# Performance work log

Hardware: AMD Instinct MI355X
Metric: run time of the kernel (lower is better)

Reference implementation:

```python
import jax, jax.numpy as jnp
import numpy as np

N, V, E, C_IN, C_OUT = 4, 4096, 2048, 64, 64


def setup_inputs() -> dict:
    key = jax.random.key(0)
    k_x, k_h, k_th = jax.random.split(key, 3)
    x = jax.random.normal(k_x, (N, V, C_IN), dtype=jnp.float32)
    H = (jax.random.uniform(k_h, (N, V, E)) < 0.05).astype(jnp.float32)
    # guarantee every vertex and every hyperedge has degree >= 1 (code divides by degree)
    v_idx = jnp.arange(V)
    H = H.at[:, v_idx, v_idx % E].set(1.0)
    # xavier_uniform for theta
    limit = float(np.sqrt(6.0 / (C_IN + C_OUT)))
    theta = jax.random.uniform(k_th, (C_IN, C_OUT), minval=-limit, maxval=limit, dtype=jnp.float32)
    bias = jnp.zeros((C_OUT,), dtype=jnp.float32)
    return {"x": x, "H": H, "theta": theta, "bias": bias}


def reference(x, H, theta, bias):
    # x: [N,V,C], H: [N,V,E] incidence, theta: [C,O], bias: [O]
    # Original builds diag_embed(1/deg) and multiplies; equivalent to direct
    # per-row / per-column scaling of H (same math, no NxVxV / NxExE diagonals).
    dv = 1.0 / H.sum(-1)            # [N,V] vertex degrees
    de = 1.0 / H.sum(1)             # [N,E] hyperedge degrees
    y = jnp.einsum('nvc,co->nvo', x, theta)          # [N,V,O]
    HDe = H * de[:, None, :]                          # H @ De  -> [N,V,E]
    y = jnp.einsum('nvc,nve->nec', y, HDe)            # vertex -> edge  [N,E,O]
    HDv = H * dv[:, :, None]                          # Dv @ H -> [N,V,E]
    y = jnp.einsum('nec,nve->nvc', y, HDv)            # edge -> vertex  [N,V,O]
    return y + bias[None, None, :]
```

## Files before the change

kernel.cpp:

```cpp
#include <hip/hip_runtime.h>
#include <hip/hip_bf16.h>
#include <stdint.h>

#define N_B 4
#define NV 4096
#define NE 2048
#define NC 64

typedef float    f32x4  __attribute__((ext_vector_type(4)));
typedef __bf16   bf16x8 __attribute__((ext_vector_type(8)));
typedef unsigned short u16;
typedef u16      u16x8  __attribute__((ext_vector_type(8)));
typedef uint32_t u32x4  __attribute__((ext_vector_type(4)));

__device__ __forceinline__ u16 f2bf_rne(float f) {
    uint32_t u = __builtin_bit_cast(uint32_t, f);
    u += 0x7FFFu + ((u >> 16) & 1u);
    return (u16)(u >> 16);
}
__device__ __forceinline__ float bf2f(u16 h) {
    uint32_t u = ((uint32_t)h) << 16;
    return __builtin_bit_cast(float, u);
}
__device__ __forceinline__ f32x4 mfma_bf16(u16x8 a, u16x8 b, f32x4 c) {
    return __builtin_amdgcn_mfma_f32_16x16x32_bf16(
        __builtin_bit_cast(bf16x8, a), __builtin_bit_cast(bf16x8, b), c, 0, 0, 0);
}
__device__ __forceinline__ u16x8 expand8(uint32_t byte) {
    u32x4 w;
#pragma unroll
    for (int p = 0; p < 4; ++p) {
        const uint32_t lo = (byte >> (2 * p)) & 1u;
        const uint32_t hi = (byte >> (2 * p + 1)) & 1u;
        w[p] = (lo | (hi << 16)) * 0x3F80u;
    }
    return __builtin_bit_cast(u16x8, w);
}

__global__ __launch_bounds__(256) void k_pack(const float* __restrict__ H,
                                              uint32_t* __restrict__ HB,
                                              uint32_t* __restrict__ HT,
                                              float* __restrict__ dvP,
                                              float* __restrict__ deP) {
    __shared__ float tile[64][65];
    const int n  = blockIdx.z;
    const int v0 = blockIdx.y * 64;
    const int e0 = blockIdx.x * 64;
    const int t = threadIdx.x, w = t >> 6, l = t & 63;

    const float* __restrict__ Hn = H + ((size_t)n * NV + v0) * NE + e0;

#pragma unroll 4
    for (int i = 0; i < 16; ++i) {
        const int row = w * 16 + i;
        const float h = Hn[(size_t)row * NE + l];
        tile[row][l] = h;
        const unsigned long long m = __ballot(h != 0.0f);
        if (l == 0)
            dvP[((size_t)blockIdx.x * N_B + n) * NV + v0 + row] = (float)__popcll(m);
        if (l < 2)
            HB[(((size_t)n * (NV / 16) + ((v0 + row) >> 4)) * (NE / 32) + (e0 >> 5) + l) * 16 +
               ((v0 + row) & 15)] = (uint32_t)(m >> (32 * l));
    }
    __syncthreads();

#pragma unroll 4
    for (int i = 0; i < 16; ++i) {
        const int col = w * 16 + i;
        const float h = tile[l][col];
        const unsigned long long m = __ballot(h != 0.0f);
        if (l == 0)
            deP[((size_t)blockIdx.y * N_B + n) * NE + e0 + col] = (float)__popcll(m);
        if (l < 2)
            HT[(((size_t)n * (NE / 16) + ((e0 + col) >> 4)) * (NV / 32) + (v0 >> 5) + l) * 16 +
               ((e0 + col) & 15)] = (uint32_t)(m >> (32 * l));
    }
}

__global__ __launch_bounds__(256) void k_deg(const float* __restrict__ dvP,
                                             const float* __restrict__ deP,
                                             float* __restrict__ dv,
                                             float* __restrict__ de) {
    const int id = blockIdx.x * 256 + threadIdx.x;
    if (id < N_B * NE) {
        float s = 0.f;
        for (int vt = 0; vt < 64; ++vt) s += deP[(size_t)vt * (N_B * NE) + id];
        de[id] = s;
    } else {
        const int j = id - N_B * NE;
        float s = 0.f;
        for (int et = 0; et < 32; ++et) s += dvP[(size_t)et * (N_B * NV) + j];
        dv[j] = s;
    }
}

__global__ __launch_bounds__(256) void k_xtheta(const float* __restrict__ x,
                                                const float* __restrict__ th,
                                                u16* __restrict__ Yh,
                                                u16* __restrict__ Yl) {
    __shared__ float xs[64][65];
    __shared__ float ts[64][65];
    const int t = threadIdx.x;
    const int n  = blockIdx.x >> 6;
    const int v0 = (blockIdx.x & 63) * 64;

#pragma unroll
    for (int i = 0; i < 4; ++i) {
        const int idx = i * 256 + t;
        const int row = idx >> 4, q = (idx & 15) * 4;
        const float4 xv = *(const float4*)&x[((size_t)(n * NV + v0 + row)) * 64 + q];
        const float4 tv = *(const float4*)&th[(size_t)row * 64 + q];
        xs[row][q] = xv.x; xs[row][q + 1] = xv.y; xs[row][q + 2] = xv.z; xs[row][q + 3] = xv.w;
        ts[row][q] = tv.x; ts[row][q + 1] = tv.y; ts[row][q + 2] = tv.z; ts[row][q + 3] = tv.w;
    }
    __syncthreads();

    const int v4 = (t & 15) * 4;
    const int c4 = (t >> 4) * 4;
    float acc[4][4] = {};
#pragma unroll
    for (int k = 0; k < 64; ++k) {
        float tv[4], xv[4];
#pragma unroll
        for (int i = 0; i < 4; ++i) { tv[i] = ts[k][c4 + i]; xv[i] = xs[v4 + i][k]; }
#pragma unroll
        for (int i = 0; i < 4; ++i)
#pragma unroll
            for (int j = 0; j < 4; ++j) acc[i][j] += tv[i] * xv[j];
    }
#pragma unroll
    for (int i = 0; i < 4; ++i) {
        ushort4 hi, lo;
        u16 h;
        h = f2bf_rne(acc[i][0]); hi.x = h; lo.x = f2bf_rne(acc[i][0] - bf2f(h));
        h = f2bf_rne(acc[i][1]); hi.y = h; lo.y = f2bf_rne(acc[i][1] - bf2f(h));
        h = f2bf_rne(acc[i][2]); hi.z = h; lo.z = f2bf_rne(acc[i][2] - bf2f(h));
        h = f2bf_rne(acc[i][3]); hi.w = h; lo.w = f2bf_rne(acc[i][3] - bf2f(h));
        const size_t o = ((size_t)n * 64 + c4 + i) * NV + v0 + v4;
        *(ushort4*)&Yh[o] = hi;
        *(ushort4*)&Yl[o] = lo;
    }
}

__global__ __launch_bounds__(256, 4) void k_v2e(const uint32_t* __restrict__ HT,
                                                const u16* __restrict__ Yh,
                                                const u16* __restrict__ Yl,
                                                float* __restrict__ P2) {
    const int n  = blockIdx.z;
    const int sp = blockIdx.y;
    const int e0 = blockIdx.x * 64;
    const int krange = NV / gridDim.y;
    const int kk0 = sp * krange;
    const int S   = krange / 32;

    const int t = threadIdx.x, w = t >> 6, l = t & 63;
    const int lq = l >> 4, lr = l & 15;
    const int sh = lq * 8;
    const int hstride = (NV / 32) * 16;

    const uint32_t* __restrict__ ht =
        HT + ((size_t)n * (NE / 16) + (e0 >> 4)) * hstride + (kk0 >> 5) * 16 + lr;
    const u16* __restrict__ ybh = Yh + ((size_t)n * 64 + w * 16 + lr) * NV + kk0 + lq * 8;
    const u16* __restrict__ ybl = Yl + ((size_t)n * 64 + w * 16 + lr) * NV + kk0 + lq * 8;

    f32x4 acc0 = {0.f,0.f,0.f,0.f}, acc1 = acc0, acc2 = acc0, acc3 = acc0;

    uint32_t A[4][4];
#pragma unroll
    for (int d = 0; d < 4; ++d) {
        A[d][0] = ht[0 * hstride + d * 16];
        A[d][1] = ht[1 * hstride + d * 16];
        A[d][2] = ht[2 * hstride + d * 16];
        A[d][3] = ht[3 * hstride + d * 16];
    }
    u16x8 BH[2], BL[2];
    BH[0] = *(const u16x8*)ybh;
    BL[0] = *(const u16x8*)ybl;

#define V2E_STEP(s, u, GUARD_A, GUARD_B)                                      \
    {                                                                         \
        const uint32_t a0 = A[u][0], a1 = A[u][1], a2 = A[u][2], a3 = A[u][3];\
        if (GUARD_A) {             \
            A[u][0] = ht[0 * hstride + ((s) + 4) * 16];                       \
            A[u][1] = ht[1 * hstride + ((s) + 4) * 16];                       \
            A[u][2] = ht[2 * hstride + ((s) + 4) * 16];                       \
            A[u][3] = ht[3 * hstride + ((s) + 4) * 16];                       \
        }                                                                     \
        if (GUARD_B) {                                                        \
            BH[((u) + 1) & 1] = *(const u16x8*)(ybh + ((s) + 1) * 32);        \
            BL[((u) + 1) & 1] = *(const u16x8*)(ybl + ((s) + 1) * 32);        \
        }                                                                     \
        const u16x8 bh = BH[(u) & 1], bl = BL[(u) & 1];                       \
        u16x8 a;                                                              \
        a = expand8((a0 >> sh) & 0xFF);                                       \
        acc0 = mfma_bf16(a, bh, acc0); acc0 = mfma_bf16(a, bl, acc0);         \
        a = expand8((a1 >> sh) & 0xFF);                                       \
        acc1 = mfma_bf16(a, bh, acc1); acc1 = mfma_bf16(a, bl, acc1);         \
        a = expand8((a2 >> sh) & 0xFF);                                       \
        acc2 = mfma_bf16(a, bh, acc2); acc2 = mfma_bf16(a, bl, acc2);         \
        a = expand8((a3 >> sh) & 0xFF);                                       \
        acc3 = mfma_bf16(a, bh, acc3); acc3 = mfma_bf16(a, bl, acc3);         \
    }

    int sb = 0;
    for (; sb < S - 4; sb += 4) {
        V2E_STEP(sb + 0, 0, true, true)
        V2E_STEP(sb + 1, 1, true, true)
        V2E_STEP(sb + 2, 2, true, true)
        V2E_STEP(sb + 3, 3, true, true)
    }
    V2E_STEP(sb + 0, 0, false, true)
    V2E_STEP(sb + 1, 1, false, true)
    V2E_STEP(sb + 2, 2, false, true)
    V2E_STEP(sb + 3, 3, false, false)
#undef V2E_STEP

    float* pb = P2 + (((size_t)sp * N_B + n) * 64 + w * 16 + lr) * NE + e0 + lq * 4;
    *(f32x4*)(pb + 0)  = acc0;
    *(f32x4*)(pb + 16) = acc1;
    *(f32x4*)(pb + 32) = acc2;
    *(f32x4*)(pb + 48) = acc3;
}

__global__ __launch_bounds__(256) void k_red2(const float* __restrict__ P2,
                                              const float* __restrict__ de,
                                              u16* __restrict__ Zh,
                                              u16* __restrict__ Zl, int nsp) {
    const int i = blockIdx.x * 256 + threadIdx.x;
    const int row = i >> 9;
    const int e4  = (i & 511) * 4;
    const int n   = row >> 6;

    float4 a = make_float4(0.f, 0.f, 0.f, 0.f);
    for (int sp = 0; sp < nsp; ++sp) {
        const float4 p = *(const float4*)&P2[((size_t)sp * 256 + row) * NE + e4];
        a.x += p.x; a.y += p.y; a.z += p.z; a.w += p.w;
    }
    const float4 d = *(const float4*)&de[(size_t)n * NE + e4];
    float z[4] = {a.x / d.x, a.y / d.y, a.z / d.z, a.w / d.w};
    ushort4 hi, lo;
    u16 h;
    h = f2bf_rne(z[0]); hi.x = h; lo.x = f2bf_rne(z[0] - bf2f(h));
    h = f2bf_rne(z[1]); hi.y = h; lo.y = f2bf_rne(z[1] - bf2f(h));
    h = f2bf_rne(z[2]); hi.z = h; lo.z = f2bf_rne(z[2] - bf2f(h));
    h = f2bf_rne(z[3]); hi.w = h; lo.w = f2bf_rne(z[3] - bf2f(h));
    *(ushort4*)&Zh[(size_t)row * NE + e4] = hi;
    *(ushort4*)&Zl[(size_t)row * NE + e4] = lo;
}

__global__ __launch_bounds__(256, 4) void k_e2v(const uint32_t* __restrict__ HB,
                                                const u16* __restrict__ Zh,
                                                const u16* __restrict__ Zl,
                                                float* __restrict__ P3) {
    const int n  = blockIdx.z;
    const int sp = blockIdx.y;
    const int v0 = blockIdx.x * 64;
    const int krange = NE / gridDim.y;
    const int kk0 = sp * krange;
    const int S   = krange / 32;

    const int t = threadIdx.x, w = t >> 6, l = t & 63;
    const int lq = l >> 4, lr = l & 15;
    const int sh = lq * 8;
    const int estride = (NE / 32) * 16;

    const uint32_t* __restrict__ hb =
        HB + ((size_t)n * (NV / 16) + (v0 >> 4)) * estride + (kk0 >> 5) * 16 + lr;
    const u16* __restrict__ zbh = Zh + ((size_t)n * 64 + w * 16 + lr) * NE + kk0 + lq * 8;
    const u16* __restrict__ zbl = Zl + ((size_t)n * 64 + w * 16 + lr) * NE + kk0 + lq * 8;

    f32x4 acc0 = {0.f,0.f,0.f,0.f}, acc1 = acc0, acc2 = acc0, acc3 = acc0;

    uint32_t A[4][4];
#pragma unroll
    for (int d = 0; d < 4; ++d) {
        A[d][0] = hb[0 * estride + d * 16];
        A[d][1] = hb[1 * estride + d * 16];
        A[d][2] = hb[2 * estride + d * 16];
        A[d][3] = hb[3 * estride + d * 16];
    }
    u16x8 BH[2], BL[2];
    BH[0] = *(const u16x8*)zbh;
    BL[0] = *(const u16x8*)zbl;

#define E2V_STEP(s, u, GUARD_A, GUARD_B)                                      \
    {                                                                         \
        const uint32_t a0 = A[u][0], a1 = A[u][1], a2 = A[u][2], a3 = A[u][3];\
        if (GUARD_A) {                                                        \
            A[u][0] = hb[0 * estride + ((s) + 4) * 16];                       \
            A[u][1] = hb[1 * estride + ((s) + 4) * 16];                       \
            A[u][2] = hb[2 * estride + ((s) + 4) * 16];                       \
            A[u][3] = hb[3 * estride + ((s) + 4) * 16];                       \
        }                                                                     \
        if (GUARD_B) {                                                        \
            BH[((u) + 1) & 1] = *(const u16x8*)(zbh + ((s) + 1) * 32);        \
            BL[((u) + 1) & 1] = *(const u16x8*)(zbl + ((s) + 1) * 32);        \
        }                                                                     \
        const u16x8 bh = BH[(u) & 1], bl = BL[(u) & 1];                       \
        u16x8 a;                                                              \
        a = expand8((a0 >> sh) & 0xFF);                                       \
        acc0 = mfma_bf16(a, bh, acc0); acc0 = mfma_bf16(a, bl, acc0);         \
        a = expand8((a1 >> sh) & 0xFF);                                       \
        acc1 = mfma_bf16(a, bh, acc1); acc1 = mfma_bf16(a, bl, acc1);         \
        a = expand8((a2 >> sh) & 0xFF);                                       \
        acc2 = mfma_bf16(a, bh, acc2); acc2 = mfma_bf16(a, bl, acc2);         \
        a = expand8((a3 >> sh) & 0xFF);                                       \
        acc3 = mfma_bf16(a, bh, acc3); acc3 = mfma_bf16(a, bl, acc3);         \
    }

    int sb = 0;
    for (; sb < S - 4; sb += 4) {
        E2V_STEP(sb + 0, 0, true, true)
        E2V_STEP(sb + 1, 1, true, true)
        E2V_STEP(sb + 2, 2, true, true)
        E2V_STEP(sb + 3, 3, true, true)
    }
    E2V_STEP(sb + 0, 0, false, true)
    E2V_STEP(sb + 1, 1, false, true)
    E2V_STEP(sb + 2, 2, false, true)
    E2V_STEP(sb + 3, 3, false, false)
#undef E2V_STEP

    float* pb = P3 + (((size_t)sp * N_B + n) * 64 + w * 16 + lr) * NV + v0 + lq * 4;
    *(f32x4*)(pb + 0)  = acc0;
    *(f32x4*)(pb + 16) = acc1;
    *(f32x4*)(pb + 32) = acc2;
    *(f32x4*)(pb + 48) = acc3;
}

__global__ __launch_bounds__(512) void k_red3(const float* __restrict__ P3,
                                              const float* __restrict__ dv,
                                              const float* __restrict__ bias,
                                              float* __restrict__ out, int nsp) {
    __shared__ float lt[64][68];
    const int n  = blockIdx.y;
    const int v0 = blockIdx.x * 64;
    const int t  = threadIdx.x;

    {
        const int c   = t >> 3;
        const int vch = (t & 7) * 8;
        float4 s0 = make_float4(0.f, 0.f, 0.f, 0.f), s1 = s0;
        for (int sp = 0; sp < nsp; ++sp) {
            const size_t base = (((size_t)sp * N_B + n) * 64 + c) * NV + v0 + vch;
            const float4 p0 = *(const float4*)&P3[base];
            const float4 p1 = *(const float4*)&P3[base + 4];
            s0.x += p0.x; s0.y += p0.y; s0.z += p0.z; s0.w += p0.w;
            s1.x += p1.x; s1.y += p1.y; s1.z += p1.z; s1.w += p1.w;
        }
        *(float4*)&lt[c][vch]     = s0;
        *(float4*)&lt[c][vch + 4] = s1;
    }
    const int vw  = t >> 3;
    const int cch = (t & 7) * 8;
    const float dsum = dv[(size_t)n * NV + v0 + vw];
    __syncthreads();

    const float rdv = 1.0f / dsum;
    const float4 b0 = *(const float4*)&bias[cch];
    const float4 b1 = *(const float4*)&bias[cch + 4];
    float4 o0, o1;
    o0.x = lt[cch + 0][vw] * rdv + b0.x;
    o0.y = lt[cch + 1][vw] * rdv + b0.y;
    o0.z = lt[cch + 2][vw] * rdv + b0.z;
    o0.w = lt[cch + 3][vw] * rdv + b0.w;
    o1.x = lt[cch + 4][vw] * rdv + b1.x;
    o1.y = lt[cch + 5][vw] * rdv + b1.y;
    o1.z = lt[cch + 6][vw] * rdv + b1.z;
    o1.w = lt[cch + 7][vw] * rdv + b1.w;
    float* dst = out + ((size_t)n * NV + v0 + vw) * 64 + cch;
    *(float4*)dst       = o0;
    *(float4*)(dst + 4) = o1;
}

extern "C" void kernel_launch(void* const* d_in, const int* in_sizes, int n_in,
                              void* d_out, int out_size, void* d_ws, size_t ws_size,
                              hipStream_t stream) {
    const float* x     = (const float*)d_in[0];
    const float* H     = (const float*)d_in[1];
    const float* theta = (const float*)d_in[2];
    const float* bias  = (const float*)d_in[3];
    float* out = (float*)d_out;

    const size_t yE   = (size_t)N_B * 64 * NV;
    const size_t zE   = (size_t)N_B * 64 * NE;
    const size_t HBW  = (size_t)N_B * (NV / 16) * (NE / 32) * 16;
    const size_t HTW  = (size_t)N_B * (NE / 16) * (NV / 32) * 16;
    const size_t depE = (size_t)64 * N_B * NE;
    const size_t dvpE = (size_t)32 * N_B * NV;
    const size_t deE  = (size_t)N_B * NE;
    const size_t dvE  = (size_t)N_B * NV;

    u16* Yh = (u16*)d_ws;
    u16* Yl = Yh + yE;
    u16* Zh = Yl + yE;
    u16* Zl = Zh + zE;
    uint32_t* HB = (uint32_t*)(Zl + zE);
    uint32_t* HT = HB + HBW;
    float* deP = (float*)(HT + HTW);
    float* dvP = deP + depE;
    float* de  = dvP + dvpE;
    float* dv  = de + deE;
    float* fbase = dv + dvE;

    const size_t fixed_bytes = (size_t)((char*)fbase - (char*)d_ws);
    const size_t avail_f = (ws_size > fixed_bytes) ? (ws_size - fixed_bytes) / 4 : 0;

    const size_t unit2 = zE;
    const size_t unit3 = yE;
    int s2 = 1, s3 = 1;
    if      (avail_f >= 8 * unit2 + 4 * unit3) { s2 = 8; s3 = 4; }
    else if (avail_f >= 4 * unit2 + 2 * unit3) { s2 = 4; s3 = 2; }
    else if (avail_f >= 2 * unit2 + 1 * unit3) { s2 = 2; s3 = 1; }

    float* P2 = fbase;
    float* P3 = P2 + (size_t)s2 * zE;

    k_pack<<<dim3(NE / 64, NV / 64, N_B), 256, 0, stream>>>(H, HB, HT, dvP, deP);
    k_xtheta<<<dim3(N_B * NV / 64), 256, 0, stream>>>(x, theta, Yh, Yl);
    k_deg<<<dim3((N_B * NE + N_B * NV) / 256), 256, 0, stream>>>(dvP, deP, dv, de);
    k_v2e<<<dim3(NE / 64, s2, N_B), 256, 0, stream>>>(HT, Yh, Yl, P2);
    k_red2<<<dim3((int)(zE / 4 / 256)), 256, 0, stream>>>(P2, de, Zh, Zl, s2);
    k_e2v<<<dim3(NV / 64, s3, N_B), 256, 0, stream>>>(HB, Zh, Zl, P3);
    k_red3<<<dim3(NV / 64, N_B), 512, 0, stream>>>(P3, dv, bias, out, s3);
}
```

Measured before the change: 106.4 us.

## Fuse all stages into one cooperative persistent kernel with grid syncs

Replaces the seven separate kernel launches with a single cooperative kernel of 1024 blocks that runs pack, x·theta, vertex-to-edge, reduction, edge-to-vertex and the final reduction, separated by grid.sync barriers. Degree partials are now accumulated with float atomics into memset buffers, which removes the separate degree-reduction kernel. The goal is to cut launch gaps and the extra partial-sum traffic. In exchange it adds grid-wide barriers, atomic contention, two memsets and a fixed work distribution, and it falls back to the multi-kernel path if a cooperative launch is not possible.

```diff
diff --git a/kernel.cpp b/kernel.cpp
--- a/kernel.cpp
+++ b/kernel.cpp
@@ -1,11 +1,11 @@
 #include <hip/hip_runtime.h>
+#include <hip/hip_cooperative_groups.h>
 #include <hip/hip_bf16.h>
 #include <stdint.h>
 
 #define N_B 4
 #define NV 4096
 #define NE 2048
-#define NC 64
 
 typedef float    f32x4  __attribute__((ext_vector_type(4)));
 typedef __bf16   bf16x8 __attribute__((ext_vector_type(8)));
@@ -37,17 +37,17 @@
     return __builtin_bit_cast(u16x8, w);
 }
 
-__global__ __launch_bounds__(256) void k_pack(const float* __restrict__ H,
+
+__device__ __forceinline__ void dev_pack_tile(const float* __restrict__ H,
                                               uint32_t* __restrict__ HB,
                                               uint32_t* __restrict__ HT,
-                                              float* __restrict__ dvP,
-                                              float* __restrict__ deP) {
-    __shared__ float tile[64][65];
-    const int n  = blockIdx.z;
-    const int v0 = blockIdx.y * 64;
-    const int e0 = blockIdx.x * 64;
-    const int t = threadIdx.x, w = t >> 6, l = t & 63;
-
+                                              float* __restrict__ dv,
+                                              float* __restrict__ de,
+                                              int tid, int t, float* smem) {
+    float (*tile)[65] = (float(*)[65])smem;
+    const int ex = tid & 31, vy = (tid >> 5) & 63, n = tid >> 11;
+    const int e0 = ex * 64, v0 = vy * 64;
+    const int w = t >> 6, l = t & 63;
     const float* __restrict__ Hn = H + ((size_t)n * NV + v0) * NE + e0;
 
 #pragma unroll 4
@@ -57,52 +57,32 @@
         tile[row][l] = h;
         const unsigned long long m = __ballot(h != 0.0f);
         if (l == 0)
-            dvP[((size_t)blockIdx.x * N_B + n) * NV + v0 + row] = (float)__popcll(m);
+            atomicAdd(&dv[(size_t)n * NV + v0 + row], (float)__popcll(m));
         if (l < 2)
             HB[(((size_t)n * (NV / 16) + ((v0 + row) >> 4)) * (NE / 32) + (e0 >> 5) + l) * 16 +
                ((v0 + row) & 15)] = (uint32_t)(m >> (32 * l));
     }
     __syncthreads();
-
 #pragma unroll 4
     for (int i = 0; i < 16; ++i) {
         const int col = w * 16 + i;
         const float h = tile[l][col];
         const unsigned long long m = __ballot(h != 0.0f);
         if (l == 0)
-            deP[((size_t)blockIdx.y * N_B + n) * NE + e0 + col] = (float)__popcll(m);
+            atomicAdd(&de[(size_t)n * NE + e0 + col], (float)__popcll(m));
         if (l < 2)
             HT[(((size_t)n * (NE / 16) + ((e0 + col) >> 4)) * (NV / 32) + (v0 >> 5) + l) * 16 +
                ((e0 + col) & 15)] = (uint32_t)(m >> (32 * l));
     }
 }
 
-__global__ __launch_bounds__(256) void k_deg(const float* __restrict__ dvP,
-                                             const float* __restrict__ deP,
-                                             float* __restrict__ dv,
-                                             float* __restrict__ de) {
-    const int id = blockIdx.x * 256 + threadIdx.x;
-    if (id < N_B * NE) {
-        float s = 0.f;
-        for (int vt = 0; vt < 64; ++vt) s += deP[(size_t)vt * (N_B * NE) + id];
-        de[id] = s;
-    } else {
-        const int j = id - N_B * NE;
-        float s = 0.f;
-        for (int et = 0; et < 32; ++et) s += dvP[(size_t)et * (N_B * NV) + j];
-        dv[j] = s;
-    }
-}
-
-__global__ __launch_bounds__(256) void k_xtheta(const float* __restrict__ x,
+__device__ __forceinline__ void dev_xtheta_tile(const float* __restrict__ x,
                                                 const float* __restrict__ th,
                                                 u16* __restrict__ Yh,
-                                                u16* __restrict__ Yl) {
-    __shared__ float xs[64][65];
-    __shared__ float ts[64][65];
-    const int t = threadIdx.x;
-    const int n  = blockIdx.x >> 6;
-    const int v0 = (blockIdx.x & 63) * 64;
+                                                u16* __restrict__ Yl,
+                                                int n, int v0, int t, float* smem) {
+    float (*xs)[65] = (float(*)[65])smem;
+    float (*ts)[65] = (float(*)[65])(smem + 64 * 65);
 
 #pragma unroll
     for (int i = 0; i < 4; ++i) {
@@ -142,18 +122,16 @@
     }
 }
 
-__global__ __launch_bounds__(256, 4) void k_v2e(const uint32_t* __restrict__ HT,
-                                                const u16* __restrict__ Yh,
-                                                const u16* __restrict__ Yl,
-                                                float* __restrict__ P2) {
-    const int n  = blockIdx.z;
-    const int sp = blockIdx.y;
-    const int e0 = blockIdx.x * 64;
-    const int krange = NV / gridDim.y;
+__device__ __forceinline__ void dev_v2e(const uint32_t* __restrict__ HT,
+                                        const u16* __restrict__ Yh,
+                                        const u16* __restrict__ Yl,
+                                        float* __restrict__ P2,
+                                        int e0, int sp, int n, int nsp, int t) {
+    const int krange = NV / nsp;
     const int kk0 = sp * krange;
     const int S   = krange / 32;
 
-    const int t = threadIdx.x, w = t >> 6, l = t & 63;
+    const int w = t >> 6, l = t & 63;
     const int lq = l >> 4, lr = l & 15;
     const int sh = lq * 8;
     const int hstride = (NV / 32) * 16;
@@ -180,7 +158,7 @@
 #define V2E_STEP(s, u, GUARD_A, GUARD_B)                                      \
     {                                                                         \
         const uint32_t a0 = A[u][0], a1 = A[u][1], a2 = A[u][2], a3 = A[u][3];\
-        if (GUARD_A) {             \
+        if (GUARD_A) {                                                        \
             A[u][0] = ht[0 * hstride + ((s) + 4) * 16];                       \
             A[u][1] = ht[1 * hstride + ((s) + 4) * 16];                       \
             A[u][2] = ht[2 * hstride + ((s) + 4) * 16];                       \
@@ -222,13 +200,12 @@
     *(f32x4*)(pb + 48) = acc3;
 }
 
-__global__ __launch_bounds__(256) void k_red2(const float* __restrict__ P2,
-                                              const float* __restrict__ de,
-                                              u16* __restrict__ Zh,
-                                              u16* __restrict__ Zl, int nsp) {
-    const int i = blockIdx.x * 256 + threadIdx.x;
-    const int row = i >> 9;
-    const int e4  = (i & 511) * 4;
+__device__ __forceinline__ void dev_red2(const float* __restrict__ P2,
+                                         const float* __restrict__ de,
+                                         u16* __restrict__ Zh,
+                                         u16* __restrict__ Zl, int id, int nsp) {
+    const int row = id >> 9;
+    const int e4  = (id & 511) * 4;
     const int n   = row >> 6;
 
     float4 a = make_float4(0.f, 0.f, 0.f, 0.f);
@@ -248,18 +225,16 @@
     *(ushort4*)&Zl[(size_t)row * NE + e4] = lo;
 }
 
-__global__ __launch_bounds__(256, 4) void k_e2v(const uint32_t* __restrict__ HB,
-                                                const u16* __restrict__ Zh,
-                                                const u16* __restrict__ Zl,
-                                                float* __restrict__ P3) {
-    const int n  = blockIdx.z;
-    const int sp = blockIdx.y;
-    const int v0 = blockIdx.x * 64;
-    const int krange = NE / gridDim.y;
+__device__ __forceinline__ void dev_e2v(const uint32_t* __restrict__ HB,
+                                        const u16* __restrict__ Zh,
+                                        const u16* __restrict__ Zl,
+                                        float* __restrict__ P3,
+                                        int v0, int sp, int n, int nsp, int t) {
+    const int krange = NE / nsp;
     const int kk0 = sp * krange;
     const int S   = krange / 32;
 
-    const int t = threadIdx.x, w = t >> 6, l = t & 63;
+    const int w = t >> 6, l = t & 63;
     const int lq = l >> 4, lr = l & 15;
     const int sh = lq * 8;
     const int estride = (NE / 32) * 16;
@@ -328,49 +303,135 @@
     *(f32x4*)(pb + 48) = acc3;
 }
 
-__global__ __launch_bounds__(512) void k_red3(const float* __restrict__ P3,
+__device__ __forceinline__ void dev_red3(const float* __restrict__ P3,
+                                         const float* __restrict__ dv,
+                                         const float* __restrict__ bias,
+                                         float* __restrict__ out,
+                                         int vtile, int n, int nsp, int t,
+                                         float* smem) {
+    float (*lt)[69] = (float(*)[69])smem;
+    const int v0 = vtile * 64;
+#pragma unroll
+    for (int q = 0; q < 4; ++q) {
+        const int f = q * 256 + t;
+        const int c = f >> 4;
+        const int vch = (f & 15) * 4;
+        float4 s = make_float4(0.f, 0.f, 0.f, 0.f);
+        for (int sp = 0; sp < nsp; ++sp) {
+            const float4 p = *(const float4*)&P3[(((size_t)sp * N_B + n) * 64 + c) * NV + v0 + vch];
+            s.x += p.x; s.y += p.y; s.z += p.z; s.w += p.w;
+        }
+        lt[c][vch] = s.x; lt[c][vch + 1] = s.y; lt[c][vch + 2] = s.z; lt[c][vch + 3] = s.w;
+    }
+    __syncthreads();
+
+    const int vw  = t >> 2;
+    const int cch = (t & 3) * 16;
+    const float rdv = 1.0f / dv[(size_t)n * NV + v0 + vw];
+    float* dst = out + ((size_t)n * NV + v0 + vw) * 64 + cch;
+#pragma unroll
+    for (int q = 0; q < 4; ++q) {
+        const float4 b = *(const float4*)&bias[cch + q * 4];
+        float4 o;
+        o.x = lt[cch + q * 4 + 0][vw] * rdv + b.x;
+        o.y = lt[cch + q * 4 + 1][vw] * rdv + b.y;
+        o.z = lt[cch + q * 4 + 2][vw] * rdv + b.z;
+        o.w = lt[cch + q * 4 + 3][vw] * rdv + b.w;
+        *(float4*)(dst + q * 4) = o;
+    }
+    __syncthreads();
+}
+
+__global__ __launch_bounds__(256, 4) void k_mega(
+    const float* __restrict__ H, const float* __restrict__ x,
+    const float* __restrict__ th,
+    uint32_t* __restrict__ HB, uint32_t* __restrict__ HT,
+    float* __restrict__ dv, float* __restrict__ de,
+    u16* __restrict__ Yh, u16* __restrict__ Yl,
+    float* __restrict__ P2, u16* __restrict__ Zh, u16* __restrict__ Zl,
+    float* __restrict__ P3, const float* __restrict__ bias,
+    float* __restrict__ out) {
+    __shared__ float smem[2 * 64 * 65];
+    const int bid = blockIdx.x;
+    const int t   = threadIdx.x;
+    cooperative_groups::grid_group grid = cooperative_groups::this_grid();
+
+    if (bid < 256) {
+        for (int i = 0; i < 5; ++i) {
+            dev_pack_tile(H, HB, HT, dv, de, bid * 5 + i, t, smem);
+            __syncthreads();
+        }
+        dev_xtheta_tile(x, th, Yh, Yl, bid >> 6, (bid & 63) * 64, t, smem);
+    } else {
+        for (int i = 0; i < 9; ++i) {
+            dev_pack_tile(H, HB, HT, dv, de, 1280 + (bid - 256) * 9 + i, t, smem);
+            __syncthreads();
+        }
+    }
+    grid.sync();
+
+    dev_v2e(HT, Yh, Yl, P2, (bid & 31) * 64, (bid >> 5) & 7, bid >> 8, 8, t);
+    grid.sync();
+
+    {
+        const int id = bid * 256 + t;
+        if (id < N_B * 64 * (NE / 4)) dev_red2(P2, de, Zh, Zl, id, 8);
+    }
+    grid.sync();
+
+    dev_e2v(HB, Zh, Zl, P3, (bid & 63) * 64, (bid >> 6) & 3, bid >> 8, 4, t);
+    grid.sync();
+
+    if (bid < 256) dev_red3(P3, dv, bias, out, bid & 63, bid >> 6, 4, t, smem);
+}
+
+__global__ __launch_bounds__(256) void k_pack(const float* __restrict__ H,
+                                              uint32_t* __restrict__ HB,
+                                              uint32_t* __restrict__ HT,
+                                              float* __restrict__ dv,
+                                              float* __restrict__ de) {
+    __shared__ float smem[64 * 65];
+    dev_pack_tile(H, HB, HT, dv, de, blockIdx.x, threadIdx.x, smem);
+}
+
+__global__ __launch_bounds__(256) void k_xtheta(const float* __restrict__ x,
+                                                const float* __restrict__ th,
+                                                u16* __restrict__ Yh,
+                                                u16* __restrict__ Yl) {
+    __shared__ float smem[2 * 64 * 65];
+    dev_xtheta_tile(x, th, Yh, Yl, blockIdx.x >> 6, (blockIdx.x & 63) * 64,
+                    threadIdx.x, smem);
+}
+
+__global__ __launch_bounds__(256, 4) void k_v2e(const uint32_t* __restrict__ HT,
+                                                const u16* __restrict__ Yh,
+                                                const u16* __restrict__ Yl,
+                                                float* __restrict__ P2) {
+    dev_v2e(HT, Yh, Yl, P2, blockIdx.x * 64, blockIdx.y, blockIdx.z,
+            gridDim.y, threadIdx.x);
+}
+
+__global__ __launch_bounds__(256) void k_red2(const float* __restrict__ P2,
+                                              const float* __restrict__ de,
+                                              u16* __restrict__ Zh,
+                                              u16* __restrict__ Zl, int nsp) {
+    dev_red2(P2, de, Zh, Zl, blockIdx.x * 256 + threadIdx.x, nsp);
+}
+
+__global__ __launch_bounds__(256, 4) void k_e2v(const uint32_t* __restrict__ HB,
+                                                const u16* __restrict__ Zh,
+                                                const u16* __restrict__ Zl,
+                                                float* __restrict__ P3) {
+    dev_e2v(HB, Zh, Zl, P3, blockIdx.x * 64, blockIdx.y, blockIdx.z,
+            gridDim.y, threadIdx.x);
+}
+
+__global__ __launch_bounds__(256) void k_red3(const float* __restrict__ P3,
                                               const float* __restrict__ dv,
                                               const float* __restrict__ bias,
                                               float* __restrict__ out, int nsp) {
-    __shared__ float lt[64][68];
-    const int n  = blockIdx.y;
-    const int v0 = blockIdx.x * 64;
-    const int t  = threadIdx.x;
-
-    {
-        const int c   = t >> 3;
-        const int vch = (t & 7) * 8;
-        float4 s0 = make_float4(0.f, 0.f, 0.f, 0.f), s1 = s0;
-        for (int sp = 0; sp < nsp; ++sp) {
-            const size_t base = (((size_t)sp * N_B + n) * 64 + c) * NV + v0 + vch;
-            const float4 p0 = *(const float4*)&P3[base];
-            const float4 p1 = *(const float4*)&P3[base + 4];
-            s0.x += p0.x; s0.y += p0.y; s0.z += p0.z; s0.w += p0.w;
-            s1.x += p1.x; s1.y += p1.y; s1.z += p1.z; s1.w += p1.w;
-        }
-        *(float4*)&lt[c][vch]     = s0;
-        *(float4*)&lt[c][vch + 4] = s1;
-    }
-    const int vw  = t >> 3;
-    const int cch = (t & 7) * 8;
-    const float dsum = dv[(size_t)n * NV + v0 + vw];
-    __syncthreads();
-
-    const float rdv = 1.0f / dsum;
-    const float4 b0 = *(const float4*)&bias[cch];
-    const float4 b1 = *(const float4*)&bias[cch + 4];
-    float4 o0, o1;
-    o0.x = lt[cch + 0][vw] * rdv + b0.x;
-    o0.y = lt[cch + 1][vw] * rdv + b0.y;
-    o0.z = lt[cch + 2][vw] * rdv + b0.z;
-    o0.w = lt[cch + 3][vw] * rdv + b0.w;
-    o1.x = lt[cch + 4][vw] * rdv + b1.x;
-    o1.y = lt[cch + 5][vw] * rdv + b1.y;
-    o1.z = lt[cch + 6][vw] * rdv + b1.z;
-    o1.w = lt[cch + 7][vw] * rdv + b1.w;
-    float* dst = out + ((size_t)n * NV + v0 + vw) * 64 + cch;
-    *(float4*)dst       = o0;
-    *(float4*)(dst + 4) = o1;
+    __shared__ float smem[64 * 69];
+    dev_red3(P3, dv, bias, out, blockIdx.x, blockIdx.y, nsp, threadIdx.x, smem);
 }
 
 extern "C" void kernel_launch(void* const* d_in, const int* in_sizes, int n_in,
@@ -382,14 +443,22 @@
     const float* bias  = (const float*)d_in[3];
     float* out = (float*)d_out;
 
-    const size_t yE   = (size_t)N_B * 64 * NV;
-    const size_t zE   = (size_t)N_B * 64 * NE;
-    const size_t HBW  = (size_t)N_B * (NV / 16) * (NE / 32) * 16;
-    const size_t HTW  = (size_t)N_B * (NE / 16) * (NV / 32) * 16;
-    const size_t depE = (size_t)64 * N_B * NE;
-    const size_t dvpE = (size_t)32 * N_B * NV;
-    const size_t deE  = (size_t)N_B * NE;
-    const size_t dvE  = (size_t)N_B * NV;
+    const size_t yE  = (size_t)N_B * 64 * NV;
+    const size_t zE  = (size_t)N_B * 64 * NE;
+    const size_t HBW = (size_t)N_B * (NV / 16) * (NE / 32) * 16;
+    const size_t HTW = (size_t)N_B * (NE / 16) * (NV / 32) * 16;
+    const size_t dvE = (size_t)N_B * NV;
+    const size_t deE = (size_t)N_B * NE;
+
+    const size_t fixed_bytes = (2 * yE + 2 * zE) * sizeof(u16) +
+                               (HBW + HTW) * sizeof(uint32_t) +
+                               (dvE + deE) * sizeof(float);
+    const size_t avail_f = (ws_size > fixed_bytes) ? (ws_size - fixed_bytes) / 4 : 0;
+
+    int s2 = 1, s3 = 1;
+    if      (avail_f >= 8 * zE + 4 * yE) { s2 = 8; s3 = 4; }
+    else if (avail_f >= 4 * zE + 2 * yE) { s2 = 4; s3 = 2; }
+    else if (avail_f >= 2 * zE + 1 * yE) { s2 = 2; s3 = 1; }
 
     u16* Yh = (u16*)d_ws;
     u16* Yl = Yh + yE;
@@ -397,30 +466,44 @@
     u16* Zl = Zh + zE;
     uint32_t* HB = (uint32_t*)(Zl + zE);
     uint32_t* HT = HB + HBW;
-    float* deP = (float*)(HT + HTW);
-    float* dvP = deP + depE;
-    float* de  = dvP + dvpE;
-    float* dv  = de + deE;
-    float* fbase = dv + dvE;
-
-    const size_t fixed_bytes = (size_t)((char*)fbase - (char*)d_ws);
-    const size_t avail_f = (ws_size > fixed_bytes) ? (ws_size - fixed_bytes) / 4 : 0;
-
-    const size_t unit2 = zE;
-    const size_t unit3 = yE;
-    int s2 = 1, s3 = 1;
-    if      (avail_f >= 8 * unit2 + 4 * unit3) { s2 = 8; s3 = 4; }
-    else if (avail_f >= 4 * unit2 + 2 * unit3) { s2 = 4; s3 = 2; }
-    else if (avail_f >= 2 * unit2 + 1 * unit3) { s2 = 2; s3 = 1; }
-
-    float* P2 = fbase;
+    float* dv = (float*)(HT + HTW);
+    float* de = dv + dvE;
+    float* P2 = de + deE;
     float* P3 = P2 + (size_t)s2 * zE;
 
-    k_pack<<<dim3(NE / 64, NV / 64, N_B), 256, 0, stream>>>(H, HB, HT, dvP, deP);
-    k_xtheta<<<dim3(N_B * NV / 64), 256, 0, stream>>>(x, theta, Yh, Yl);
-    k_deg<<<dim3((N_B * NE + N_B * NV) / 256), 256, 0, stream>>>(dvP, deP, dv, de);
-    k_v2e<<<dim3(NE / 64, s2, N_B), 256, 0, stream>>>(HT, Yh, Yl, P2);
-    k_red2<<<dim3((int)(zE / 4 / 256)), 256, 0, stream>>>(P2, de, Zh, Zl, s2);
-    k_e2v<<<dim3(NV / 64, s3, N_B), 256, 0, stream>>>(HB, Zh, Zl, P3);
-    k_red3<<<dim3(NV / 64, N_B), 512, 0, stream>>>(P3, dv, bias, out, s3);
-}
+    hipMemsetAsync(dv, 0, dvE * sizeof(float), stream);
+    hipMemsetAsync(de, 0, deE * sizeof(float), stream);
+
+    bool use_mega = (s2 == 8 && s3 == 4);
+    if (use_mega) {
+        int dev = 0;
+        hipGetDevice(&dev);
+        int coop = 0;
+        hipDeviceGetAttribute(&coop, hipDeviceAttributeCooperativeLaunch, dev);
+        int ncu = 0;
+        hipDeviceGetAttribute(&ncu, hipDeviceAttributeMultiprocessorCount, dev);
+        int maxb = 0;
+        hipOccupancyMaxActiveBlocksPerMultiprocessor(&maxb, (const void*)k_mega, 256, 0);
+        use_mega = coop && ncu > 0 && (size_t)maxb * (size_t)ncu >= 1024;
+    }
+
+    bool launched = false;
+    if (use_mega) {
+        void* args[] = {
+            (void*)&H, (void*)&x, (void*)&theta,
+            (void*)&HB, (void*)&HT, (void*)&dv, (void*)&de,
+            (void*)&Yh, (void*)&Yl, (void*)&P2, (void*)&Zh, (void*)&Zl,
+            (void*)&P3, (void*)&bias, (void*)&out};
+        launched = hipLaunchCooperativeKernel((const void*)k_mega, dim3(1024),
+                                              dim3(256), args, 0, stream) == hipSuccess;
+    }
+
+    if (!launched) {
+        k_xtheta<<<dim3(N_B * NV / 64), 256, 0, stream>>>(x, theta, Yh, Yl);
+        k_pack<<<dim3((NE / 64) * (NV / 64) * N_B), 256, 0, stream>>>(H, HB, HT, dv, de);
+        k_v2e<<<dim3(NE / 64, s2, N_B), 256, 0, stream>>>(HT, Yh, Yl, P2);
+        k_red2<<<dim3((int)(zE / 4 / 256)), 256, 0, stream>>>(P2, de, Zh, Zl, s2);
+        k_e2v<<<dim3(NV / 64, s3, N_B), 256, 0, stream>>>(HB, Zh, Zl, P3);
+        k_red3<<<dim3(NV / 64, N_B), 256, 0, stream>>>(P3, dv, bias, out, s3);
+    }
+}
```

After: 244.3 us. 130% more time.

## Merge front kernels, fold degree reduction into v2e, raise split-K and occupancy

Applied to the files above, without the earlier changes.

Combines the H packing and x·theta kernels into one launch selected by block index, and moves the degree reduction into the first threads of the v2e kernel, cutting two launches. The v2e and e2v kernels get a higher occupancy bound (8 waves per SIMD target), a shallower A prefetch depth (2 instead of 4) to save registers, and an XCD-aware block remapping. The split-K factors double when workspace allows. The risks are a longer partial-sum reduction and less latency hiding from the shallower prefetch.

```diff
diff --git a/kernel.cpp b/kernel.cpp
--- a/kernel.cpp
+++ b/kernel.cpp
@@ -5,7 +5,6 @@
 #define N_B 4
 #define NV 4096
 #define NE 2048
-#define NC 64
 
 typedef float    f32x4  __attribute__((ext_vector_type(4)));
 typedef __bf16   bf16x8 __attribute__((ext_vector_type(8)));
@@ -37,123 +36,133 @@
     return __builtin_bit_cast(u16x8, w);
 }
 
-__global__ __launch_bounds__(256) void k_pack(const float* __restrict__ H,
-                                              uint32_t* __restrict__ HB,
-                                              uint32_t* __restrict__ HT,
-                                              float* __restrict__ dvP,
-                                              float* __restrict__ deP) {
-    __shared__ float tile[64][65];
-    const int n  = blockIdx.z;
-    const int v0 = blockIdx.y * 64;
-    const int e0 = blockIdx.x * 64;
-    const int t = threadIdx.x, w = t >> 6, l = t & 63;
-
-    const float* __restrict__ Hn = H + ((size_t)n * NV + v0) * NE + e0;
+__global__ __launch_bounds__(256) void k_front(const float* __restrict__ H,
+                                               const float* __restrict__ x,
+                                               const float* __restrict__ th,
+                                               uint32_t* __restrict__ HB,
+                                               uint32_t* __restrict__ HT,
+                                               float* __restrict__ dvP,
+                                               float* __restrict__ deP,
+                                               u16* __restrict__ Yh,
+                                               u16* __restrict__ Yl) {
+    __shared__ float smem[2 * 64 * 65];
+    const int bid = blockIdx.x;
+    const int t = threadIdx.x;
+
+    if (bid < 8192) {
+        float (*tile)[65] = (float(*)[65])smem;
+        const int ex = bid & 31, vy = (bid >> 5) & 63, n = bid >> 11;
+        const int e0 = ex * 64, v0 = vy * 64;
+        const int w = t >> 6, l = t & 63;
+        const float* __restrict__ Hn = H + ((size_t)n * NV + v0) * NE + e0;
 
 #pragma unroll 4
-    for (int i = 0; i < 16; ++i) {
-        const int row = w * 16 + i;
-        const float h = Hn[(size_t)row * NE + l];
-        tile[row][l] = h;
-        const unsigned long long m = __ballot(h != 0.0f);
-        if (l == 0)
-            dvP[((size_t)blockIdx.x * N_B + n) * NV + v0 + row] = (float)__popcll(m);
-        if (l < 2)
-            HB[(((size_t)n * (NV / 16) + ((v0 + row) >> 4)) * (NE / 32) + (e0 >> 5) + l) * 16 +
-               ((v0 + row) & 15)] = (uint32_t)(m >> (32 * l));
-    }
-    __syncthreads();
-
+        for (int i = 0; i < 16; ++i) {
+            const int row = w * 16 + i;
+            const float h = Hn[(size_t)row * NE + l];
+            tile[row][l] = h;
+            const unsigned long long m = __ballot(h != 0.0f);
+            if (l == 0)
+                dvP[((size_t)ex * N_B + n) * NV + v0 + row] = (float)__popcll(m);
+            if (l < 2)
+                HB[(((size_t)n * (NV / 16) + ((v0 + row) >> 4)) * (NE / 32) + (e0 >> 5) + l) * 16 +
+                   ((v0 + row) & 15)] = (uint32_t)(m >> (32 * l));
+        }
+        __syncthreads();
 #pragma unroll 4
-    for (int i = 0; i < 16; ++i) {
-        const int col = w * 16 + i;
-        const float h = tile[l][col];
-        const unsigned long long m = __ballot(h != 0.0f);
-        if (l == 0)
-            deP[((size_t)blockIdx.y * N_B + n) * NE + e0 + col] = (float)__popcll(m);
-        if (l < 2)
-            HT[(((size_t)n * (NE / 16) + ((e0 + col) >> 4)) * (NV / 32) + (v0 >> 5) + l) * 16 +
-               ((e0 + col) & 15)] = (uint32_t)(m >> (32 * l));
-    }
-}
-
-__global__ __launch_bounds__(256) void k_deg(const float* __restrict__ dvP,
-                                             const float* __restrict__ deP,
-                                             float* __restrict__ dv,
-                                             float* __restrict__ de) {
-    const int id = blockIdx.x * 256 + threadIdx.x;
-    if (id < N_B * NE) {
-        float s = 0.f;
-        for (int vt = 0; vt < 64; ++vt) s += deP[(size_t)vt * (N_B * NE) + id];
-        de[id] = s;
+        for (int i = 0; i < 16; ++i) {
+            const int col = w * 16 + i;
+            const float h = tile[l][col];
+            const unsigned long long m = __ballot(h != 0.0f);
+            if (l == 0)
+                deP[((size_t)vy * N_B + n) * NE + e0 + col] = (float)__popcll(m);
+            if (l < 2)
+                HT[(((size_t)n * (NE / 16) + ((e0 + col) >> 4)) * (NV / 32) + (v0 >> 5) + l) * 16 +
+                   ((e0 + col) & 15)] = (uint32_t)(m >> (32 * l));
+        }
     } else {
-        const int j = id - N_B * NE;
-        float s = 0.f;
-        for (int et = 0; et < 32; ++et) s += dvP[(size_t)et * (N_B * NV) + j];
-        dv[j] = s;
-    }
-}
-
-__global__ __launch_bounds__(256) void k_xtheta(const float* __restrict__ x,
-                                                const float* __restrict__ th,
-                                                u16* __restrict__ Yh,
-                                                u16* __restrict__ Yl) {
-    __shared__ float xs[64][65];
-    __shared__ float ts[64][65];
-    const int t = threadIdx.x;
-    const int n  = blockIdx.x >> 6;
-    const int v0 = (blockIdx.x & 63) * 64;
-
-#pragma unroll
-    for (int i = 0; i < 4; ++i) {
-        const int idx = i * 256 + t;
-        const int row = idx >> 4, q = (idx & 15) * 4;
-        const float4 xv = *(const float4*)&x[((size_t)(n * NV + v0 + row)) * 64 + q];
-        const float4 tv = *(const float4*)&th[(size_t)row * 64 + q];
-        xs[row][q] = xv.x; xs[row][q + 1] = xv.y; xs[row][q + 2] = xv.z; xs[row][q + 3] = xv.w;
-        ts[row][q] = tv.x; ts[row][q + 1] = tv.y; ts[row][q + 2] = tv.z; ts[row][q + 3] = tv.w;
-    }
-    __syncthreads();
-
-    const int v4 = (t & 15) * 4;
-    const int c4 = (t >> 4) * 4;
-    float acc[4][4] = {};
-#pragma unroll
-    for (int k = 0; k < 64; ++k) {
-        float tv[4], xv[4];
-#pragma unroll
-        for (int i = 0; i < 4; ++i) { tv[i] = ts[k][c4 + i]; xv[i] = xs[v4 + i][k]; }
-#pragma unroll
-        for (int i = 0; i < 4; ++i)
-#pragma unroll
-            for (int j = 0; j < 4; ++j) acc[i][j] += tv[i] * xv[j];
-    }
-#pragma unroll
-    for (int i = 0; i < 4; ++i) {
-        ushort4 hi, lo;
-        u16 h;
-        h = f2bf_rne(acc[i][0]); hi.x = h; lo.x = f2bf_rne(acc[i][0] - bf2f(h));
-        h = f2bf_rne(acc[i][1]); hi.y = h; lo.y = f2bf_rne(acc[i][1] - bf2f(h));
-        h = f2bf_rne(acc[i][2]); hi.z = h; lo.z = f2bf_rne(acc[i][2] - bf2f(h));
-        h = f2bf_rne(acc[i][3]); hi.w = h; lo.w = f2bf_rne(acc[i][3] - bf2f(h));
-        const size_t o = ((size_t)n * 64 + c4 + i) * NV + v0 + v4;
-        *(ushort4*)&Yh[o] = hi;
-        *(ushort4*)&Yl[o] = lo;
-    }
-}
-
-__global__ __launch_bounds__(256, 4) void k_v2e(const uint32_t* __restrict__ HT,
+        float (*xs)[65] = (float(*)[65])smem;
+        float (*ts)[65] = (float(*)[65])(smem + 64 * 65);
+        const int bx = bid - 8192;
+        const int n = bx >> 6, v0 = (bx & 63) * 64;
+
+#pragma unroll
+        for (int i = 0; i < 4; ++i) {
+            const int idx = i * 256 + t;
+            const int row = idx >> 4, q = (idx & 15) * 4;
+            const float4 xv = *(const float4*)&x[((size_t)(n * NV + v0 + row)) * 64 + q];
+            const float4 tv = *(const float4*)&th[(size_t)row * 64 + q];
+            xs[row][q] = xv.x; xs[row][q + 1] = xv.y; xs[row][q + 2] = xv.z; xs[row][q + 3] = xv.w;
+            ts[row][q] = tv.x; ts[row][q + 1] = tv.y; ts[row][q + 2] = tv.z; ts[row][q + 3] = tv.w;
+        }
+        __syncthreads();
+
+        const int v4 = (t & 15) * 4;
+        const int c4 = (t >> 4) * 4;
+        float acc[4][4] = {};
+#pragma unroll
+        for (int k = 0; k < 64; ++k) {
+            float tv[4], xv[4];
+#pragma unroll
+            for (int i = 0; i < 4; ++i) { tv[i] = ts[k][c4 + i]; xv[i] = xs[v4 + i][k]; }
+#pragma unroll
+            for (int i = 0; i < 4; ++i)
+#pragma unroll
+                for (int j = 0; j < 4; ++j) acc[i][j] += tv[i] * xv[j];
+        }
+#pragma unroll
+        for (int i = 0; i < 4; ++i) {
+            ushort4 hi, lo;
+            u16 h;
+            h = f2bf_rne(acc[i][0]); hi.x = h; lo.x = f2bf_rne(acc[i][0] - bf2f(h));
+            h = f2bf_rne(acc[i][1]); hi.y = h; lo.y = f2bf_rne(acc[i][1] - bf2f(h));
+            h = f2bf_rne(acc[i][2]); hi.z = h; lo.z = f2bf_rne(acc[i][2] - bf2f(h));
+            h = f2bf_rne(acc[i][3]); hi.w = h; lo.w = f2bf_rne(acc[i][3] - bf2f(h));
+            const size_t o = ((size_t)n * 64 + c4 + i) * NV + v0 + v4;
+            *(ushort4*)&Yh[o] = hi;
+            *(ushort4*)&Yl[o] = lo;
+        }
+    }
+}
+
+__global__ __launch_bounds__(256, 8) void k_v2e(const uint32_t* __restrict__ HT,
                                                 const u16* __restrict__ Yh,
                                                 const u16* __restrict__ Yl,
-                                                float* __restrict__ P2) {
-    const int n  = blockIdx.z;
-    const int sp = blockIdx.y;
-    const int e0 = blockIdx.x * 64;
-    const int krange = NV / gridDim.y;
+                                                float* __restrict__ P2,
+                                                const float* __restrict__ deP,
+                                                const float* __restrict__ dvP,
+                                                float* __restrict__ de,
+                                                float* __restrict__ dv) {
+    const int t = threadIdx.x;
+    const int s2 = gridDim.y;
+    const int lin = blockIdx.x + 32 * (blockIdx.y + s2 * blockIdx.z);
+    const int nb = 32 * s2 * N_B;
+
+    if (t < 64) {
+        const int id = lin * 64 + t;
+        if (id < N_B * NE) {
+            float s = 0.f;
+            for (int vt = 0; vt < 64; ++vt) s += deP[(size_t)vt * (N_B * NE) + id];
+            de[id] = s;
+        } else if (id < N_B * NE + N_B * NV) {
+            const int j = id - N_B * NE;
+            float s = 0.f;
+            for (int et = 0; et < 32; ++et) s += dvP[(size_t)et * (N_B * NV) + j];
+            dv[j] = s;
+        }
+    }
+
+    const int wid = (lin & 7) * (nb >> 3) + (lin >> 3);
+    const int n   = wid / (32 * s2);
+    const int rem = wid % (32 * s2);
+    const int sp  = rem >> 5;
+    const int e0  = (rem & 31) * 64;
+
+    const int krange = NV / s2;
     const int kk0 = sp * krange;
     const int S   = krange / 32;
 
-    const int t = threadIdx.x, w = t >> 6, l = t & 63;
+    const int w = t >> 6, l = t & 63;
     const int lq = l >> 4, lr = l & 15;
     const int sh = lq * 8;
     const int hstride = (NV / 32) * 16;
@@ -165,9 +174,9 @@
 
     f32x4 acc0 = {0.f,0.f,0.f,0.f}, acc1 = acc0, acc2 = acc0, acc3 = acc0;
 
-    uint32_t A[4][4];
-#pragma unroll
-    for (int d = 0; d < 4; ++d) {
+    uint32_t A[2][4];
+#pragma unroll
+    for (int d = 0; d < 2; ++d) {
         A[d][0] = ht[0 * hstride + d * 16];
         A[d][1] = ht[1 * hstride + d * 16];
         A[d][2] = ht[2 * hstride + d * 16];
@@ -177,20 +186,20 @@
     BH[0] = *(const u16x8*)ybh;
     BL[0] = *(const u16x8*)ybl;
 
-#define V2E_STEP(s, u, GUARD_A, GUARD_B)                                      \
+#define V2E_STEP(s, u, GA, GB)                                                \
     {                                                                         \
         const uint32_t a0 = A[u][0], a1 = A[u][1], a2 = A[u][2], a3 = A[u][3];\
-        if (GUARD_A) {             \
-            A[u][0] = ht[0 * hstride + ((s) + 4) * 16];                       \
-            A[u][1] = ht[1 * hstride + ((s) + 4) * 16];                       \
-            A[u][2] = ht[2 * hstride + ((s) + 4) * 16];                       \
-            A[u][3] = ht[3 * hstride + ((s) + 4) * 16];                       \
+        if (GA) {                                                             \
+            A[u][0] = ht[0 * hstride + ((s) + 2) * 16];                       \
+            A[u][1] = ht[1 * hstride + ((s) + 2) * 16];                       \
+            A[u][2] = ht[2 * hstride + ((s) + 2) * 16];                       \
+            A[u][3] = ht[3 * hstride + ((s) + 2) * 16];                       \
         }                                                                     \
-        if (GUARD_B) {                                                        \
+        if (GB) {                                                             \
             BH[((u) + 1) & 1] = *(const u16x8*)(ybh + ((s) + 1) * 32);        \
             BL[((u) + 1) & 1] = *(const u16x8*)(ybl + ((s) + 1) * 32);        \
         }                                                                     \
-        const u16x8 bh = BH[(u) & 1], bl = BL[(u) & 1];                       \
+        const u16x8 bh = BH[u], bl = BL[u];                                   \
         u16x8 a;                                                              \
         a = expand8((a0 >> sh) & 0xFF);                                       \
         acc0 = mfma_bf16(a, bh, acc0); acc0 = mfma_bf16(a, bl, acc0);         \
@@ -203,16 +212,12 @@
     }
 
     int sb = 0;
-    for (; sb < S - 4; sb += 4) {
+    for (; sb < S - 2; sb += 2) {
         V2E_STEP(sb + 0, 0, true, true)
         V2E_STEP(sb + 1, 1, true, true)
-        V2E_STEP(sb + 2, 2, true, true)
-        V2E_STEP(sb + 3, 3, true, true)
     }
     V2E_STEP(sb + 0, 0, false, true)
-    V2E_STEP(sb + 1, 1, false, true)
-    V2E_STEP(sb + 2, 2, false, true)
-    V2E_STEP(sb + 3, 3, false, false)
+    V2E_STEP(sb + 1, 1, false, false)
 #undef V2E_STEP
 
     float* pb = P2 + (((size_t)sp * N_B + n) * 64 + w * 16 + lr) * NE + e0 + lq * 4;
@@ -248,18 +253,26 @@
     *(ushort4*)&Zl[(size_t)row * NE + e4] = lo;
 }
 
-__global__ __launch_bounds__(256, 4) void k_e2v(const uint32_t* __restrict__ HB,
+__global__ __launch_bounds__(256, 8) void k_e2v(const uint32_t* __restrict__ HB,
                                                 const u16* __restrict__ Zh,
                                                 const u16* __restrict__ Zl,
                                                 float* __restrict__ P3) {
-    const int n  = blockIdx.z;
-    const int sp = blockIdx.y;
-    const int v0 = blockIdx.x * 64;
-    const int krange = NE / gridDim.y;
+    const int t = threadIdx.x;
+    const int s3 = gridDim.y;
+    const int lin = blockIdx.x + 64 * (blockIdx.y + s3 * blockIdx.z);
+    const int nb = 64 * s3 * N_B;
+
+    const int wid = (lin & 7) * (nb >> 3) + (lin >> 3);
+    const int n   = wid / (64 * s3);
+    const int rem = wid % (64 * s3);
+    const int sp  = rem >> 6;
+    const int v0  = (rem & 63) * 64;
+
+    const int krange = NE / s3;
     const int kk0 = sp * krange;
     const int S   = krange / 32;
 
-    const int t = threadIdx.x, w = t >> 6, l = t & 63;
+    const int w = t >> 6, l = t & 63;
     const int lq = l >> 4, lr = l & 15;
     const int sh = lq * 8;
     const int estride = (NE / 32) * 16;
@@ -271,9 +284,9 @@
 
     f32x4 acc0 = {0.f,0.f,0.f,0.f}, acc1 = acc0, acc2 = acc0, acc3 = acc0;
 
-    uint32_t A[4][4];
-#pragma unroll
-    for (int d = 0; d < 4; ++d) {
+    uint32_t A[2][4];
+#pragma unroll
+    for (int d = 0; d < 2; ++d) {
         A[d][0] = hb[0 * estride + d * 16];
         A[d][1] = hb[1 * estride + d * 16];
         A[d][2] = hb[2 * estride + d * 16];
@@ -283,20 +296,20 @@
     BH[0] = *(const u16x8*)zbh;
     BL[0] = *(const u16x8*)zbl;
 
-#define E2V_STEP(s, u, GUARD_A, GUARD_B)                                      \
+#define E2V_STEP(s, u, GA, GB)                                                \
     {                                                                         \
         const uint32_t a0 = A[u][0], a1 = A[u][1], a2 = A[u][2], a3 = A[u][3];\
-        if (GUARD_A) {                                                        \
-            A[u][0] = hb[0 * estride + ((s) + 4) * 16];                       \
-            A[u][1] = hb[1 * estride + ((s) + 4) * 16];                       \
-            A[u][2] = hb[2 * estride + ((s) + 4) * 16];                       \
-            A[u][3] = hb[3 * estride + ((s) + 4) * 16];                       \
+        if (GA) {                                                             \
+            A[u][0] = hb[0 * estride + ((s) + 2) * 16];                       \
+            A[u][1] = hb[1 * estride + ((s) + 2) * 16];                       \
+            A[u][2] = hb[2 * estride + ((s) + 2) * 16];                       \
+            A[u][3] = hb[3 * estride + ((s) + 2) * 16];                       \
         }                                                                     \
-        if (GUARD_B) {                                                        \
+        if (GB) {                                                             \
             BH[((u) + 1) & 1] = *(const u16x8*)(zbh + ((s) + 1) * 32);        \
             BL[((u) + 1) & 1] = *(const u16x8*)(zbl + ((s) + 1) * 32);        \
         }                                                                     \
-        const u16x8 bh = BH[(u) & 1], bl = BL[(u) & 1];                       \
+        const u16x8 bh = BH[u], bl = BL[u];                                   \
         u16x8 a;                                                              \
         a = expand8((a0 >> sh) & 0xFF);                                       \
         acc0 = mfma_bf16(a, bh, acc0); acc0 = mfma_bf16(a, bl, acc0);         \
@@ -309,16 +322,12 @@
     }
 
     int sb = 0;
-    for (; sb < S - 4; sb += 4) {
+    for (; sb < S - 2; sb += 2) {
         E2V_STEP(sb + 0, 0, true, true)
         E2V_STEP(sb + 1, 1, true, true)
-        E2V_STEP(sb + 2, 2, true, true)
-        E2V_STEP(sb + 3, 3, true, true)
     }
     E2V_STEP(sb + 0, 0, false, true)
-    E2V_STEP(sb + 1, 1, false, true)
-    E2V_STEP(sb + 2, 2, false, true)
-    E2V_STEP(sb + 3, 3, false, false)
+    E2V_STEP(sb + 1, 1, false, false)
 #undef E2V_STEP
 
     float* pb = P3 + (((size_t)sp * N_B + n) * 64 + w * 16 + lr) * NV + v0 + lq * 4;
@@ -406,20 +415,16 @@
     const size_t fixed_bytes = (size_t)((char*)fbase - (char*)d_ws);
     const size_t avail_f = (ws_size > fixed_bytes) ? (ws_size - fixed_bytes) / 4 : 0;
 
-    const size_t unit2 = zE;
-    const size_t unit3 = yE;
-    int s2 = 1, s3 = 1;
-    if      (avail_f >= 8 * unit2 + 4 * unit3) { s2 = 8; s3 = 4; }
-    else if (avail_f >= 4 * unit2 + 2 * unit3) { s2 = 4; s3 = 2; }
-    else if (avail_f >= 2 * unit2 + 1 * unit3) { s2 = 2; s3 = 1; }
+    int s2 = 2, s3 = 1;
+    if      (avail_f >= 16 * zE + 8 * yE) { s2 = 16; s3 = 8; }
+    else if (avail_f >=  8 * zE + 4 * yE) { s2 = 8;  s3 = 4; }
+    else if (avail_f >=  4 * zE + 2 * yE) { s2 = 4;  s3 = 2; }
 
     float* P2 = fbase;
     float* P3 = P2 + (size_t)s2 * zE;
 
-    k_pack<<<dim3(NE / 64, NV / 64, N_B), 256, 0, stream>>>(H, HB, HT, dvP, deP);
-    k_xtheta<<<dim3(N_B * NV / 64), 256, 0, stream>>>(x, theta, Yh, Yl);
-    k_deg<<<dim3((N_B * NE + N_B * NV) / 256), 256, 0, stream>>>(dvP, deP, dv, de);
-    k_v2e<<<dim3(NE / 64, s2, N_B), 256, 0, stream>>>(HT, Yh, Yl, P2);
+    k_front<<<dim3(8192 + 256), 256, 0, stream>>>(H, x, theta, HB, HT, dvP, deP, Yh, Yl);
+    k_v2e<<<dim3(NE / 64, s2, N_B), 256, 0, stream>>>(HT, Yh, Yl, P2, deP, dvP, de, dv);
     k_red2<<<dim3((int)(zE / 4 / 256)), 256, 0, stream>>>(P2, de, Zh, Zl, s2);
     k_e2v<<<dim3(NV / 64, s3, N_B), 256, 0, stream>>>(HB, Zh, Zl, P3);
     k_red3<<<dim3(NV / 64, N_B), 512, 0, stream>>>(P3, dv, bias, out, s3);
```

Result: slower. 155.6 us (+46.2%).
